# Optimization experiments

Measured on AMD Instinct MI355X. Metric: run time of the kernel, lower is better.

The kernel has to match this reference:

```python
import jax, jax.numpy as jnp
import numpy as np

N = 64          # num_nodes (EEG electrodes)
T = 200         # time steps
B = 64          # batch
H = 64          # hidden_dim
K = 3           # cheb_k
F_IN = 1        # input_dim
D_GRU = 2 * H * N  # 8192, GRU input size


def setup_inputs() -> dict:
    key = jax.random.key(0)
    ks = jax.random.split(key, 24)
    s = 0.05
    inp = {
        "x": jax.random.normal(ks[0], (B, N, T), dtype=jnp.float32),
        "spatial_ei": jax.random.randint(ks[1], (2, 512), 0, N, dtype=jnp.int32),
        "spatial_ew": jax.random.uniform(ks[2], (512,), dtype=jnp.float32),
        "functional_ei": jax.random.randint(ks[3], (2, 1024), 0, N, dtype=jnp.int32),
        "functional_ew": jax.random.uniform(ks[4], (1024,), dtype=jnp.float32),
        # ChebConv: K separate Linear(F_IN->H, bias shared once)
        "Wcheb": jax.random.normal(ks[5], (K, F_IN, H), dtype=jnp.float32) * s,
        "bcheb": jnp.zeros((H,), jnp.float32),
        # GCNConv
        "Wgcn": jax.random.normal(ks[6], (F_IN, H), dtype=jnp.float32) * s,
        "bgcn": jnp.zeros((H,), jnp.float32),
        # bidirectional GRU (torch layout: gates r,z,n stacked -> 3H rows)
        "Wih_f": jax.random.normal(ks[7], (3 * H, D_GRU), dtype=jnp.float32) * s,
        "Whh_f": jax.random.normal(ks[8], (3 * H, H), dtype=jnp.float32) * s,
        "bih_f": jnp.zeros((3 * H,), jnp.float32),
        "bhh_f": jnp.zeros((3 * H,), jnp.float32),
        "Wih_b": jax.random.normal(ks[9], (3 * H, D_GRU), dtype=jnp.float32) * s,
        "Whh_b": jax.random.normal(ks[10], (3 * H, H), dtype=jnp.float32) * s,
        "bih_b": jnp.zeros((3 * H,), jnp.float32),
        "bhh_b": jnp.zeros((3 * H,), jnp.float32),
        # attention + classifier heads
        "attn_W": jax.random.normal(ks[11], (2 * H, 1), dtype=jnp.float32) * s,
        "attn_b": jnp.zeros((1,), jnp.float32),
        "clf_W": jax.random.normal(ks[12], (2 * H, 1), dtype=jnp.float32) * s,
        "clf_b": jnp.zeros((1,), jnp.float32),
    }
    return inp


def _gru_scan(xp, Whh, bhh, reverse):
    # xp: [B, T, 3H] precomputed input projection; returns [B, T, H]
    xp_t = jnp.swapaxes(xp, 0, 1)  # [T, B, 3H]
    Hh = Whh.shape[1]

    def step(h, xg):
        hg = h @ Whh.T + bhh
        xr, xz, xn = jnp.split(xg, 3, axis=-1)
        hr, hz, hn = jnp.split(hg, 3, axis=-1)
        r = jax.nn.sigmoid(xr + hr)
        z = jax.nn.sigmoid(xz + hz)
        n = jnp.tanh(xn + r * hn)
        h_new = (1.0 - z) * n + z * h
        return h_new, h_new

    h0 = jnp.zeros((xp.shape[0], Hh), xp.dtype)
    _, hs = jax.lax.scan(step, h0, xp_t, reverse=reverse)
    return jnp.swapaxes(hs, 0, 1)


def _forward(x, spatial_ei, spatial_ew, functional_ei, functional_ew,
             Wcheb, bcheb, Wgcn, bgcn,
             Wih_f, Whh_f, bih_f, bhh_f, Wih_b, Whh_b, bih_b, bhh_b,
             attn_W, attn_b, clf_W, clf_b):
    x = x[..., None]  # [B, N, T, 1] (the x.dim()==3 -> unsqueeze path)
    Bsz, Nn, Tt, _ = x.shape

    # ---- ChebConv (PyG, sym norm, lambda_max=2): L_tilde = -D^-1/2 A D^-1/2
    # (scaled-Laplacian self loops cancel: 2*1/2 - 1 = 0)
    row, col = spatial_ei[0], spatial_ei[1]
    deg = jax.ops.segment_sum(spatial_ew, row, num_segments=Nn)
    dinv = jnp.where(deg > 0, jax.lax.rsqrt(jnp.where(deg > 0, deg, 1.0)), 0.0)
    wn = dinv[row] * spatial_ew * dinv[col]
    # operator S[i, j]: aggregate source j into target i (source_to_target flow)
    S = jnp.zeros((Nn, Nn), x.dtype).at[col, row].add(wn)
    Ltil = -S
    Tx0 = x
    Tx1 = jnp.einsum('ij,bjtf->bitf', Ltil, Tx0)
    out_s = jnp.einsum('bntf,fh->bnth', Tx0, Wcheb[0]) + jnp.einsum('bntf,fh->bnth', Tx1, Wcheb[1])
    for k in range(2, K):
        Tx2 = 2.0 * jnp.einsum('ij,bjtf->bitf', Ltil, Tx1) - Tx0
        out_s = out_s + jnp.einsum('bntf,fh->bnth', Tx2, Wcheb[k])
        Tx0, Tx1 = Tx1, Tx2
    h_sp = out_s + bcheb  # [B, N, T, H]

    # ---- GCNConv (PyG gcn_norm with self loops, weight 1)
    row, col = functional_ei[0], functional_ei[1]
    deg = jax.ops.segment_sum(functional_ew, col, num_segments=Nn) + 1.0
    dinv = jax.lax.rsqrt(deg)
    wn = dinv[row] * functional_ew * dinv[col]
    Sg = jnp.zeros((Nn, Nn), x.dtype).at[col, row].add(wn) + jnp.diag(dinv * dinv)
    h_fn = jnp.einsum('bntf,fh->bnth', jnp.einsum('ij,bjtf->bitf', Sg, x), Wgcn) + bgcn

    # ---- stack over time, flatten nodes
    h = jnp.concatenate([h_sp, h_fn], axis=-1)           # [B, N, T, 2H]
    gru_in = jnp.transpose(h, (0, 2, 1, 3)).reshape(Bsz, Tt, Nn * 2 * H)

    # ---- bidirectional GRU
    xp_f = jnp.einsum('btd,gd->btg', gru_in, Wih_f) + bih_f
    xp_b = jnp.einsum('btd,gd->btg', gru_in, Wih_b) + bih_b
    h_f = _gru_scan(xp_f, Whh_f, bhh_f, reverse=False)
    h_b = _gru_scan(xp_b, Whh_b, bhh_b, reverse=True)
    gru_out = jnp.concatenate([h_f, h_b], axis=-1)       # [B, T, 2H]

    # ---- attention pooling + classifier
    scores = jnp.tanh(gru_out @ attn_W + attn_b)         # [B, T, 1]
    aw = jax.nn.softmax(scores, axis=1)
    ctx = jnp.sum(aw * gru_out, axis=1)                  # [B, 2H]
    return jax.nn.sigmoid(ctx @ clf_W + clf_b)           # [B, 1]


def reference(x, spatial_ei, spatial_ew, functional_ei, functional_ew,
              Wcheb, bcheb, Wgcn, bgcn,
              Wih_f, Whh_f, bih_f, bhh_f, Wih_b, Whh_b, bih_b, bhh_b,
              attn_W, attn_b, clf_W, clf_b):
    return _forward(x, spatial_ei, spatial_ew, functional_ei, functional_ew,
                    Wcheb, bcheb, Wgcn, bgcn,
                    Wih_f, Whh_f, bih_f, bhh_f, Wih_b, Whh_b, bih_b, bhh_b,
                    attn_W, attn_b, clf_W, clf_b)
```

## Files before the change

### kernel.cpp

```cpp
#include <hip/hip_runtime.h>
#include <math.h>

#define Nn 64
#define Tt 200
#define Bb 64

__device__ __forceinline__ float sigm(float x){ return 1.0f/(1.0f+__expf(-x)); }
__device__ __forceinline__ float tanh_fast(float x){
  x = fminf(fmaxf(x, -15.f), 15.f);
  float e = __expf(-2.f*x);
  return (1.f - e)/(1.f + e);
}

typedef __attribute__((ext_vector_type(2))) _Float16 h2v;
typedef __attribute__((ext_vector_type(4))) float f4;

#if __has_builtin(__builtin_amdgcn_fdot2)
#define DOT2(w,hv,acc) __builtin_amdgcn_fdot2((w),(hv),(acc),false)
#else
#define DOT2(w,hv,acc) fmaf((float)(w)[0],(float)(hv)[0], fmaf((float)(w)[1],(float)(hv)[1],(acc)))
#endif

__global__ __launch_bounds__(256) void k1_graphs(
    const int* __restrict__ sp_ei, const float* __restrict__ sp_ew,
    const int* __restrict__ fn_ei, const float* __restrict__ fn_ew,
    float* __restrict__ Lg, float* __restrict__ L2g, float* __restrict__ Gm)
{
  __shared__ float deg[Nn];
  __shared__ float dinv[Nn];
  __shared__ float S[64*68];
  const int tid = threadIdx.x;

  if (tid < Nn) deg[tid] = 0.f;
  for (int i=tid;i<64*68;i+=256) S[i]=0.f;
  __syncthreads();
  for (int e=tid;e<512;e+=256) atomicAdd(&deg[sp_ei[e]], sp_ew[e]);
  __syncthreads();
  if (tid < Nn) dinv[tid] = (deg[tid] > 0.f) ? rsqrtf(deg[tid]) : 0.f;
  __syncthreads();
  for (int e=tid;e<512;e+=256) {
    int r = sp_ei[e], c = sp_ei[512+e];
    atomicAdd(&S[c*68 + r], dinv[r]*sp_ew[e]*dinv[c]);
  }
  __syncthreads();
  for (int i=tid;i<4096;i+=256) Lg[i] = -S[(i>>6)*68 + (i&63)];
  {
    const int n = tid>>2, mb = (tid&3)*16;
    float a[16];
    #pragma unroll
    for (int q=0;q<16;q++) a[q]=0.f;
    for (int j=0;j<64;j++){
      float snj = S[n*68+j];
      const float4* rj = (const float4*)&S[j*68+mb];
      #pragma unroll
      for (int q=0;q<4;q++){
        float4 v = rj[q];
        a[q*4+0]=fmaf(snj,v.x,a[q*4+0]);
        a[q*4+1]=fmaf(snj,v.y,a[q*4+1]);
        a[q*4+2]=fmaf(snj,v.z,a[q*4+2]);
        a[q*4+3]=fmaf(snj,v.w,a[q*4+3]);
      }
    }
    #pragma unroll
    for (int q=0;q<16;q++){
      int m = mb+q;
      L2g[n*64+m] = 2.f*a[q] - (n==m ? 1.f : 0.f);
    }
  }
  __syncthreads();

  if (tid < Nn) deg[tid] = 0.f;
  for (int i=tid;i<64*68;i+=256) S[i]=0.f;
  __syncthreads();
  for (int e=tid;e<1024;e+=256) atomicAdd(&deg[fn_ei[1024+e]], fn_ew[e]);
  __syncthreads();
  if (tid < Nn) dinv[tid] = rsqrtf(deg[tid] + 1.f);
  __syncthreads();
  for (int e=tid;e<1024;e+=256) {
    int r = fn_ei[e], c = fn_ei[1024+e];
    atomicAdd(&S[c*68 + r], dinv[r]*fn_ew[e]*dinv[c]);
  }
  __syncthreads();
  if (tid < Nn) S[tid*68 + tid] += dinv[tid]*dinv[tid];
  __syncthreads();
  for (int i=tid;i<4096;i+=256) Gm[i] = S[(i>>6)*68 + (i&63)];
}

__global__ __launch_bounds__(64) void k2_aeff(
    const float* __restrict__ Wih_f, const float* __restrict__ bih_f,
    const float* __restrict__ Wih_b, const float* __restrict__ bih_b,
    const float* __restrict__ Wcheb, const float* __restrict__ bcheb,
    const float* __restrict__ Wgcn,  const float* __restrict__ bgcn,
    const float* __restrict__ Lg, const float* __restrict__ L2g,
    const float* __restrict__ Gm,
    float* __restrict__ Aeff, float* __restrict__ constv)
{
  const int g = blockIdx.x;
  const int dir = (g >= 192) ? 1 : 0;
  const int grow = dir ? g - 192 : g;
  const float* Wih = dir ? Wih_b : Wih_f;
  const float* bih = dir ? bih_b : bih_f;

  __shared__ float wrow[64*129];
  __shared__ float arow[256];
  const int tid = threadIdx.x;

  for (int i = tid; i < 8192; i += 64)
    wrow[(i>>7)*129 + (i&127)] = Wih[grow*8192 + i];
  __syncthreads();

  const int n = tid;
  float a0=0.f,a1=0.f,a2=0.f,a3=0.f,cp=0.f;
  for (int c=0;c<64;c++) {
    float w1 = wrow[n*129 + c];
    a0 = fmaf(w1, Wcheb[c],     a0);
    a1 = fmaf(w1, Wcheb[64+c],  a1);
    a2 = fmaf(w1, Wcheb[128+c], a2);
    cp = fmaf(w1, bcheb[c],     cp);
    float w2 = wrow[n*129 + 64 + c];
    a3 = fmaf(w2, Wgcn[c], a3);
    cp = fmaf(w2, bgcn[c], cp);
  }
  arow[n*4+0]=a0; arow[n*4+1]=a1; arow[n*4+2]=a2; arow[n*4+3]=a3;
  for (int off=32; off; off>>=1) cp += __shfl_down(cp, off, 64);
  if (tid==0) constv[g] = cp + bih[grow];
  __syncthreads();

  const int m = tid;
  float ae = arow[m*4+0];
  for (int nn2=0; nn2<64; nn2++) {
    ae = fmaf(arow[nn2*4+1], Lg [nn2*64+m], ae);
    ae = fmaf(arow[nn2*4+2], L2g[nn2*64+m], ae);
    ae = fmaf(arow[nn2*4+3], Gm [nn2*64+m], ae);
  }
  Aeff[g*64+m] = ae;
}

__global__ __launch_bounds__(256) void k4_gemm(
    const float* __restrict__ x, const float* __restrict__ Aeff,
    const float* __restrict__ constv, float* __restrict__ xp)
{
  const int m0 = blockIdx.x*64, g0 = blockIdx.y*64;
  __shared__ float sX[64*68];
  __shared__ float sA[64*68];
  const int tid = threadIdx.x;

  {
    const int row = tid & 63;
    const int kq  = tid >> 6;
    const int m = m0 + row;
    const int b = m / 200;
    const int t = m - b*200;
    const float* xb = x + (size_t)b*64*200 + t;
    #pragma unroll
    for (int kk=0; kk<16; ++kk) {
      int k = kq*16 + kk;
      sX[k*68 + row] = xb[(size_t)k*200];
    }
  }
  {
    const float4* A4 = (const float4*)Aeff;
    #pragma unroll
    for (int i=0;i<4;i++) {
      int f = tid + i*256;
      int r2 = f >> 4, kq2 = f & 15;
      float4 w = A4[(g0+r2)*16 + kq2];
      sA[(kq2*4+0)*68 + r2] = w.x;
      sA[(kq2*4+1)*68 + r2] = w.y;
      sA[(kq2*4+2)*68 + r2] = w.z;
      sA[(kq2*4+3)*68 + r2] = w.w;
    }
  }
  __syncthreads();

  const int tm = tid & 15, tn = tid >> 4;
  float acc[4][4] = {};
  #pragma unroll 8
  for (int k=0;k<64;k++) {
    float4 a  = *(const float4*)&sX[k*68 + tm*4];
    float4 bb = *(const float4*)&sA[k*68 + tn*4];
    float av[4]={a.x,a.y,a.z,a.w}, bv[4]={bb.x,bb.y,bb.z,bb.w};
    #pragma unroll
    for (int i=0;i<4;i++)
      #pragma unroll
      for (int j=0;j<4;j++)
        acc[i][j] = fmaf(av[i], bv[j], acc[i][j]);
  }

  float cv[4];
  #pragma unroll
  for (int j=0;j<4;j++) cv[j] = constv[g0 + tn*4 + j];
  #pragma unroll
  for (int i=0;i<4;i++) {
    int mrow = m0 + tm*4 + i;
    #pragma unroll
    for (int j=0;j<4;j++)
      xp[mrow*384 + g0 + tn*4 + j] = acc[i][j] + cv[j];
  }
}

__global__ __launch_bounds__(64)
__attribute__((amdgpu_waves_per_eu(1, 1)))
void k5_gru(
    const float* __restrict__ xp,
    const float* __restrict__ Whh_f, const float* __restrict__ bhh_f,
    const float* __restrict__ Whh_b, const float* __restrict__ bhh_b,
    float* __restrict__ gru_out)
{
  const int bd = blockIdx.x;
  const int b = bd >> 1, dir = bd & 1;
  const int g = threadIdx.x & 63;
  const float* Whh = dir ? Whh_b : Whh_f;
  const float* bhh = dir ? bhh_b : bhh_f;

  h2v wr[32], wz[32], wn[32];
  #pragma unroll
  for (int i=0;i<32;i++){
    float2 a = ((const float2*)(Whh + (size_t)g*64))[i];
    float2 bq= ((const float2*)(Whh + (size_t)(64+g)*64))[i];
    float2 c = ((const float2*)(Whh + (size_t)(128+g)*64))[i];
    wr[i] = h2v{(_Float16)a.x, (_Float16)a.y};
    wz[i] = h2v{(_Float16)bq.x,(_Float16)bq.y};
    wn[i] = h2v{(_Float16)c.x, (_Float16)c.y};
  }
  const float br_ = bhh[g], bz_ = bhh[64+g], bn_ = bhh[128+g];

  __shared__ __align__(16) _Float16 hsh[64];
  hsh[g] = (_Float16)0.f;

  const int t0 = dir ? (Tt-1) : 0;
  const int tstep = dir ? -1 : 1;
  const float* xb = xp + (size_t)(b*Tt)*384 + dir*192 + g;
  float* gout = gru_out + (size_t)(b*Tt)*128 + dir*64 + g;

  float h = 0.f;
  float xrA = xb[(size_t)t0*384], xzA = xb[(size_t)t0*384+64], xnA = xb[(size_t)t0*384+128];
  const int t1 = t0 + tstep;
  float xrB = xb[(size_t)t1*384], xzB = xb[(size_t)t1*384+64], xnB = xb[(size_t)t1*384+128];

  int t = t0;
  auto STEP = [&](float& xr, float& xz, float& xn){
    const float cxr = xr, cxz = xz, cxn = xn;
    const int tpre = t + 2*tstep;
    if ((unsigned)tpre < (unsigned)Tt) {
      xr = xb[(size_t)tpre*384];
      xz = xb[(size_t)tpre*384+64];
      xn = xb[(size_t)tpre*384+128];
    }

    const uint4* hp4 = (const uint4*)hsh;
    union U { uint4 v; h2v p[4]; };
    float ar0=0.f,ar1=0.f,az0=0.f,az1=0.f,an0=0.f,an1=0.f;

#define DOTS8(U0,U1,base)                                                     \
    { _Pragma("unroll")                                                       \
      for (int j=0;j<4;j++){                                                  \
        ar0=DOT2(wr[(base)+j],  U0.p[j],ar0);                                 \
        az0=DOT2(wz[(base)+j],  U0.p[j],az0);                                 \
        an0=DOT2(wn[(base)+j],  U0.p[j],an0);                                 \
        ar1=DOT2(wr[(base)+4+j],U1.p[j],ar1);                                 \
        az1=DOT2(wz[(base)+4+j],U1.p[j],az1);                                 \
        an1=DOT2(wn[(base)+4+j],U1.p[j],an1);                                 \
      } }

    U A0,A1,B0,B1,C0,C1,D0,D1;
    A0.v=hp4[0]; A1.v=hp4[1]; B0.v=hp4[2]; B1.v=hp4[3];
    __builtin_amdgcn_sched_group_barrier(0x100, 4, 0);
    DOTS8(A0,A1,0);
    __builtin_amdgcn_sched_group_barrier(0x2, 24, 0);
    C0.v=hp4[4]; C1.v=hp4[5];
    __builtin_amdgcn_sched_group_barrier(0x100, 2, 0);
    DOTS8(B0,B1,8);
    __builtin_amdgcn_sched_group_barrier(0x2, 24, 0);
    D0.v=hp4[6]; D1.v=hp4[7];
    __builtin_amdgcn_sched_group_barrier(0x100, 2, 0);
    DOTS8(C0,C1,16);
    __builtin_amdgcn_sched_group_barrier(0x2, 24, 0);
    DOTS8(D0,D1,24);
    __builtin_amdgcn_sched_group_barrier(0x2, 24, 0);
#undef DOTS8

    float r   = sigm(cxr + (ar0+ar1) + br_);
    float z   = sigm(cxz + (az0+az1) + bz_);
    float nn2 = tanh_fast(cxn + r*((an0+an1) + bn_));
    float hnew = (1.f - z)*nn2 + z*h;
    h = hnew;
    hsh[g] = (_Float16)hnew;
    gout[(size_t)t*128] = hnew;
    t += tstep;
  };

  for (int sp=0; sp<Tt; sp+=2) { STEP(xrA,xzA,xnA); STEP(xrB,xzB,xnB); }
}

__global__ __launch_bounds__(256) void k6_attn(
    const float* __restrict__ gru_out,
    const float* __restrict__ attn_W, const float* __restrict__ attn_b,
    const float* __restrict__ clf_W,  const float* __restrict__ clf_b,
    float* __restrict__ out)
{
  const int b = blockIdx.x, tid = threadIdx.x;
  __shared__ float s_s[Tt];
  __shared__ float red[256];
  __shared__ float aW[128], cW[128];
  if (tid < 128) { aW[tid]=attn_W[tid]; cW[tid]=clf_W[tid]; }
  __syncthreads();

  if (tid < Tt) {
    const float* row = gru_out + (b*Tt + tid)*128;
    float acc = 0.f;
    for (int j=0;j<128;j++) acc = fmaf(row[j], aW[j], acc);
    s_s[tid] = tanhf(acc + attn_b[0]);
  }
  __syncthreads();

  red[tid] = (tid < Tt) ? s_s[tid] : -1e30f;
  __syncthreads();
  for (int s2=128;s2;s2>>=1){ if(tid<s2) red[tid]=fmaxf(red[tid],red[tid+s2]); __syncthreads(); }
  float mx = red[0];
  __syncthreads();

  float e = 0.f;
  if (tid < Tt) { e = expf(s_s[tid]-mx); s_s[tid] = e; }
  red[tid] = e;
  __syncthreads();
  for (int s2=128;s2;s2>>=1){ if(tid<s2) red[tid]+=red[tid+s2]; __syncthreads(); }
  float total = red[0];
  __syncthreads();

  float p = 0.f;
  if (tid < 128) {
    float c = 0.f;
    for (int t=0;t<Tt;t++) c = fmaf(s_s[t], gru_out[(b*Tt+t)*128 + tid], c);
    p = (c/total)*cW[tid];
  }
  red[tid] = p;
  __syncthreads();
  for (int s2=128;s2;s2>>=1){ if(tid<s2) red[tid]+=red[tid+s2]; __syncthreads(); }
  if (tid==0) out[b] = sigm(red[0] + clf_b[0]);
}

extern "C" void kernel_launch(void* const* d_in, const int* in_sizes, int n_in,
                              void* d_out, int out_size, void* d_ws, size_t ws_size,
                              hipStream_t stream)
{
  const float* x      = (const float*)d_in[0];
  const int*   sp_ei  = (const int*)  d_in[1];
  const float* sp_ew  = (const float*)d_in[2];
  const int*   fn_ei  = (const int*)  d_in[3];
  const float* fn_ew  = (const float*)d_in[4];
  const float* Wcheb  = (const float*)d_in[5];
  const float* bcheb  = (const float*)d_in[6];
  const float* Wgcn   = (const float*)d_in[7];
  const float* bgcn   = (const float*)d_in[8];
  const float* Wih_f  = (const float*)d_in[9];
  const float* Whh_f  = (const float*)d_in[10];
  const float* bih_f  = (const float*)d_in[11];
  const float* bhh_f  = (const float*)d_in[12];
  const float* Wih_b  = (const float*)d_in[13];
  const float* Whh_b  = (const float*)d_in[14];
  const float* bih_b  = (const float*)d_in[15];
  const float* bhh_b  = (const float*)d_in[16];
  const float* attn_W = (const float*)d_in[17];
  const float* attn_b = (const float*)d_in[18];
  const float* clf_W  = (const float*)d_in[19];
  const float* clf_b  = (const float*)d_in[20];
  float* out = (float*)d_out;

  float* ws     = (float*)d_ws;
  float* Lg     = ws;
  float* L2g    = Lg   + 4096;
  float* Gm     = L2g  + 4096;
  float* Aeff   = Gm   + 4096;
  float* constv = Aeff + 24576;
  float* xp     = constv + 512;
  float* gro    = xp   + 4915200;

  hipLaunchKernelGGL(k1_graphs,    dim3(1),      dim3(256), 0, stream,
                     sp_ei, sp_ew, fn_ei, fn_ew, Lg, L2g, Gm);
  hipLaunchKernelGGL(k2_aeff,      dim3(384),    dim3(64),  0, stream,
                     Wih_f, bih_f, Wih_b, bih_b, Wcheb, bcheb, Wgcn, bgcn,
                     Lg, L2g, Gm, Aeff, constv);
  hipLaunchKernelGGL(k4_gemm,      dim3(200, 6), dim3(256), 0, stream,
                     x, Aeff, constv, xp);
  hipLaunchKernelGGL(k5_gru,       dim3(128),    dim3(64),  0, stream,
                     xp, Whh_f, bhh_f, Whh_b, bhh_b, gro);
  hipLaunchKernelGGL(k6_attn,      dim3(64),     dim3(256), 0, stream,
                     gro, attn_W, attn_b, clf_W, clf_b, out);
}
```

Baseline: 136.9 us.

## Fuse forward and backward GRU directions into one wave per batch

The recurrent kernel now processes both GRU directions for a batch element in a single 64-thread block, holding both directions' hidden weights in registers and interleaving their dot products and gate math each step. This halves the grid and gives the scheduler two independent recurrence chains to overlap, targeting the serial latency of each timestep. It doubles register pressure and per-step instruction count, and it removes the custom sched_group_barrier ordering.

```diff
diff --git a/kernel.cpp b/kernel.cpp
--- a/kernel.cpp
+++ b/kernel.cpp
@@ -207,90 +207,98 @@
     const float* __restrict__ Whh_b, const float* __restrict__ bhh_b,
     float* __restrict__ gru_out)
 {
-  const int bd = blockIdx.x;
-  const int b = bd >> 1, dir = bd & 1;
+  const int b = blockIdx.x;
   const int g = threadIdx.x & 63;
-  const float* Whh = dir ? Whh_b : Whh_f;
-  const float* bhh = dir ? bhh_b : bhh_f;
-
-  h2v wr[32], wz[32], wn[32];
+
+  h2v wrF[32], wzF[32], wnF[32], wrB[32], wzB[32], wnB[32];
   #pragma unroll
   for (int i=0;i<32;i++){
-    float2 a = ((const float2*)(Whh + (size_t)g*64))[i];
-    float2 bq= ((const float2*)(Whh + (size_t)(64+g)*64))[i];
-    float2 c = ((const float2*)(Whh + (size_t)(128+g)*64))[i];
-    wr[i] = h2v{(_Float16)a.x, (_Float16)a.y};
-    wz[i] = h2v{(_Float16)bq.x,(_Float16)bq.y};
-    wn[i] = h2v{(_Float16)c.x, (_Float16)c.y};
-  }
-  const float br_ = bhh[g], bz_ = bhh[64+g], bn_ = bhh[128+g];
-
-  __shared__ __align__(16) _Float16 hsh[64];
-  hsh[g] = (_Float16)0.f;
-
-  const int t0 = dir ? (Tt-1) : 0;
-  const int tstep = dir ? -1 : 1;
-  const float* xb = xp + (size_t)(b*Tt)*384 + dir*192 + g;
-  float* gout = gru_out + (size_t)(b*Tt)*128 + dir*64 + g;
-
-  float h = 0.f;
-  float xrA = xb[(size_t)t0*384], xzA = xb[(size_t)t0*384+64], xnA = xb[(size_t)t0*384+128];
-  const int t1 = t0 + tstep;
-  float xrB = xb[(size_t)t1*384], xzB = xb[(size_t)t1*384+64], xnB = xb[(size_t)t1*384+128];
-
-  int t = t0;
-  auto STEP = [&](float& xr, float& xz, float& xn){
-    const float cxr = xr, cxz = xz, cxn = xn;
-    const int tpre = t + 2*tstep;
-    if ((unsigned)tpre < (unsigned)Tt) {
-      xr = xb[(size_t)tpre*384];
-      xz = xb[(size_t)tpre*384+64];
-      xn = xb[(size_t)tpre*384+128];
-    }
-
-    const uint4* hp4 = (const uint4*)hsh;
+    float2 a = ((const float2*)(Whh_f + (size_t)g*64))[i];
+    float2 c = ((const float2*)(Whh_f + (size_t)(64+g)*64))[i];
+    float2 d = ((const float2*)(Whh_f + (size_t)(128+g)*64))[i];
+    wrF[i] = h2v{(_Float16)a.x, (_Float16)a.y};
+    wzF[i] = h2v{(_Float16)c.x, (_Float16)c.y};
+    wnF[i] = h2v{(_Float16)d.x, (_Float16)d.y};
+    float2 a2 = ((const float2*)(Whh_b + (size_t)g*64))[i];
+    float2 c2 = ((const float2*)(Whh_b + (size_t)(64+g)*64))[i];
+    float2 d2 = ((const float2*)(Whh_b + (size_t)(128+g)*64))[i];
+    wrB[i] = h2v{(_Float16)a2.x, (_Float16)a2.y};
+    wzB[i] = h2v{(_Float16)c2.x, (_Float16)c2.y};
+    wnB[i] = h2v{(_Float16)d2.x, (_Float16)d2.y};
+  }
+  const float brF = bhh_f[g], bzF = bhh_f[64+g], bnF = bhh_f[128+g];
+  const float brB = bhh_b[g], bzB = bhh_b[64+g], bnB = bhh_b[128+g];
+
+  __shared__ __align__(16) _Float16 hshF[64];
+  __shared__ __align__(16) _Float16 hshB[64];
+  hshF[g] = (_Float16)0.f;
+  hshB[g] = (_Float16)0.f;
+
+  const float* xbF = xp + (size_t)(b*Tt)*384 + g;
+  const float* xbB = xp + (size_t)(b*Tt)*384 + 192 + g;
+  float* goF = gru_out + (size_t)(b*Tt)*128 + g;
+  float* goB = gru_out + (size_t)(b*Tt)*128 + 64 + g;
+
+  float hF = 0.f, hB = 0.f;
+  float xrFA = xbF[0],            xzFA = xbF[64],            xnFA = xbF[128];
+  float xrFB = xbF[384],          xzFB = xbF[384+64],        xnFB = xbF[384+128];
+  float xrBA = xbB[(size_t)199*384], xzBA = xbB[(size_t)199*384+64], xnBA = xbB[(size_t)199*384+128];
+  float xrBB = xbB[(size_t)198*384], xzBB = xbB[(size_t)198*384+64], xnBB = xbB[(size_t)198*384+128];
+
+  int tF = 0, tB = Tt-1;
+  auto STEP = [&](float& xrF, float& xzF, float& xnF,
+                  float& xrB, float& xzB, float& xnB){
+    const float cxrF=xrF, cxzF=xzF, cxnF=xnF;
+    const float cxrB=xrB, cxzB=xzB, cxnB=xnB;
+    const int tpF = tF + 2, tpB = tB - 2;
+    if (tpF < Tt) {
+      xrF = xbF[(size_t)tpF*384]; xzF = xbF[(size_t)tpF*384+64]; xnF = xbF[(size_t)tpF*384+128];
+    }
+    if (tpB >= 0) {
+      xrB = xbB[(size_t)tpB*384]; xzB = xbB[(size_t)tpB*384+64]; xnB = xbB[(size_t)tpB*384+128];
+    }
+
+    const uint4* hF4 = (const uint4*)hshF;
+    const uint4* hB4 = (const uint4*)hshB;
     union U { uint4 v; h2v p[4]; };
-    float ar0=0.f,ar1=0.f,az0=0.f,az1=0.f,an0=0.f,an1=0.f;
-
-#define DOTS8(U0,U1,base)                                                     \
-    { _Pragma("unroll")                                                       \
-      for (int j=0;j<4;j++){                                                  \
-        ar0=DOT2(wr[(base)+j],  U0.p[j],ar0);                                 \
-        az0=DOT2(wz[(base)+j],  U0.p[j],az0);                                 \
-        an0=DOT2(wn[(base)+j],  U0.p[j],an0);                                 \
-        ar1=DOT2(wr[(base)+4+j],U1.p[j],ar1);                                 \
-        az1=DOT2(wz[(base)+4+j],U1.p[j],az1);                                 \
-        an1=DOT2(wn[(base)+4+j],U1.p[j],an1);                                 \
-      } }
-
-    U A0,A1,B0,B1,C0,C1,D0,D1;
-    A0.v=hp4[0]; A1.v=hp4[1]; B0.v=hp4[2]; B1.v=hp4[3];
-    __builtin_amdgcn_sched_group_barrier(0x100, 4, 0);
-    DOTS8(A0,A1,0);
-    __builtin_amdgcn_sched_group_barrier(0x2, 24, 0);
-    C0.v=hp4[4]; C1.v=hp4[5];
-    __builtin_amdgcn_sched_group_barrier(0x100, 2, 0);
-    DOTS8(B0,B1,8);
-    __builtin_amdgcn_sched_group_barrier(0x2, 24, 0);
-    D0.v=hp4[6]; D1.v=hp4[7];
-    __builtin_amdgcn_sched_group_barrier(0x100, 2, 0);
-    DOTS8(C0,C1,16);
-    __builtin_amdgcn_sched_group_barrier(0x2, 24, 0);
-    DOTS8(D0,D1,24);
-    __builtin_amdgcn_sched_group_barrier(0x2, 24, 0);
-#undef DOTS8
-
-    float r   = sigm(cxr + (ar0+ar1) + br_);
-    float z   = sigm(cxz + (az0+az1) + bz_);
-    float nn2 = tanh_fast(cxn + r*((an0+an1) + bn_));
-    float hnew = (1.f - z)*nn2 + z*h;
-    h = hnew;
-    hsh[g] = (_Float16)hnew;
-    gout[(size_t)t*128] = hnew;
-    t += tstep;
+    float arF0=0.f,arF1=0.f,azF0=0.f,azF1=0.f,anF0=0.f,anF1=0.f;
+    float arB0=0.f,arB1=0.f,azB0=0.f,azB1=0.f,anB0=0.f,anB1=0.f;
+
+    #pragma unroll
+    for (int c=0;c<4;c++){
+      U F0,F1,B0,B1;
+      F0.v = hF4[2*c]; F1.v = hF4[2*c+1];
+      B0.v = hB4[2*c]; B1.v = hB4[2*c+1];
+      const int base = 8*c;
+      #pragma unroll
+      for (int j=0;j<4;j++){
+        arF0=DOT2(wrF[base+j],  F0.p[j],arF0); azF0=DOT2(wzF[base+j],  F0.p[j],azF0); anF0=DOT2(wnF[base+j],  F0.p[j],anF0);
+        arB0=DOT2(wrB[base+j],  B0.p[j],arB0); azB0=DOT2(wzB[base+j],  B0.p[j],azB0); anB0=DOT2(wnB[base+j],  B0.p[j],anB0);
+        arF1=DOT2(wrF[base+4+j],F1.p[j],arF1); azF1=DOT2(wzF[base+4+j],F1.p[j],azF1); anF1=DOT2(wnF[base+4+j],F1.p[j],anF1);
+        arB1=DOT2(wrB[base+4+j],B1.p[j],arB1); azB1=DOT2(wzB[base+4+j],B1.p[j],azB1); anB1=DOT2(wnB[base+4+j],B1.p[j],anB1);
+      }
+    }
+
+    float rF  = sigm(cxrF + (arF0+arF1) + brF);
+    float rB  = sigm(cxrB + (arB0+arB1) + brB);
+    float zF  = sigm(cxzF + (azF0+azF1) + bzF);
+    float zB  = sigm(cxzB + (azB0+azB1) + bzB);
+    float nF  = tanh_fast(cxnF + rF*((anF0+anF1) + bnF));
+    float nB  = tanh_fast(cxnB + rB*((anB0+anB1) + bnB));
+    float hnF = (1.f - zF)*nF + zF*hF;
+    float hnB = (1.f - zB)*nB + zB*hB;
+    hF = hnF; hB = hnB;
+    hshF[g] = (_Float16)hnF;
+    hshB[g] = (_Float16)hnB;
+    goF[(size_t)tF*128] = hnF;
+    goB[(size_t)tB*128] = hnB;
+    tF++; tB--;
   };
 
-  for (int sp=0; sp<Tt; sp+=2) { STEP(xrA,xzA,xnA); STEP(xrB,xzB,xnB); }
+  for (int sp=0; sp<Tt; sp+=2) {
+    STEP(xrFA,xzFA,xnFA, xrBA,xzBA,xnBA);
+    STEP(xrFB,xzFB,xnFB, xrBB,xzBB,xnBB);
+  }
 }
 
 __global__ __launch_bounds__(256) void k6_attn(
@@ -383,7 +391,7 @@
                      Lg, L2g, Gm, Aeff, constv);
   hipLaunchKernelGGL(k4_gemm,      dim3(200, 6), dim3(256), 0, stream,
                      x, Aeff, constv, xp);
-  hipLaunchKernelGGL(k5_gru,       dim3(128),    dim3(64),  0, stream,
+  hipLaunchKernelGGL(k5_gru,       dim3(64),     dim3(64),  0, stream,
                      xp, Whh_f, bhh_f, Whh_b, bhh_b, gro);
   hipLaunchKernelGGL(k6_attn,      dim3(64),     dim3(256), 0, stream,
                      gro, attn_W, attn_b, clf_W, clf_b, out);
```

Measured after the change: 242.6 us. +77.3%, slower.

## Process two batch sequences per GRU wavefront to interleave independent recurrences

Applied to the files above, without the earlier changes.

Each GRU block now runs two batch elements for the same direction, with separate shared-memory hidden-state buffers, and the grid is halved from 128 to 64 blocks. The two independent recurrences are interleaved in one instruction stream so their dot-product and activation latencies can overlap within a wave, and the register-held weights are reused for both. The explicit sched_group_barrier scheduling hints are dropped. In exchange, per-step instruction count doubles per wave and fewer CUs are used, so the serial step time may grow.

```diff
diff --git a/kernel.cpp b/kernel.cpp
--- a/kernel.cpp
+++ b/kernel.cpp
@@ -207,8 +207,9 @@
     const float* __restrict__ Whh_b, const float* __restrict__ bhh_b,
     float* __restrict__ gru_out)
 {
-  const int bd = blockIdx.x;
-  const int b = bd >> 1, dir = bd & 1;
+  const int bid = blockIdx.x;
+  const int dir = bid & 1;
+  const int b0 = (bid >> 1)*2, b1 = b0 + 1;
   const int g = threadIdx.x & 63;
   const float* Whh = dir ? Whh_b : Whh_f;
   const float* bhh = dir ? bhh_b : bhh_f;
@@ -225,72 +226,77 @@
   }
   const float br_ = bhh[g], bz_ = bhh[64+g], bn_ = bhh[128+g];
 
-  __shared__ __align__(16) _Float16 hsh[64];
-  hsh[g] = (_Float16)0.f;
+  __shared__ __align__(16) _Float16 h0sh[64];
+  __shared__ __align__(16) _Float16 h1sh[64];
+  h0sh[g] = (_Float16)0.f;
+  h1sh[g] = (_Float16)0.f;
 
   const int t0 = dir ? (Tt-1) : 0;
   const int tstep = dir ? -1 : 1;
-  const float* xb = xp + (size_t)(b*Tt)*384 + dir*192 + g;
-  float* gout = gru_out + (size_t)(b*Tt)*128 + dir*64 + g;
-
-  float h = 0.f;
-  float xrA = xb[(size_t)t0*384], xzA = xb[(size_t)t0*384+64], xnA = xb[(size_t)t0*384+128];
-  const int t1 = t0 + tstep;
-  float xrB = xb[(size_t)t1*384], xzB = xb[(size_t)t1*384+64], xnB = xb[(size_t)t1*384+128];
+  const float* xb0 = xp + (size_t)(b0*Tt)*384 + dir*192 + g;
+  const float* xb1 = xp + (size_t)(b1*Tt)*384 + dir*192 + g;
+  float* go0 = gru_out + (size_t)(b0*Tt)*128 + dir*64 + g;
+  float* go1 = gru_out + (size_t)(b1*Tt)*128 + dir*64 + g;
+
+  float h0 = 0.f, h1 = 0.f;
+  const int t1i = t0 + tstep;
+  float x0rA = xb0[(size_t)t0*384],  x0zA = xb0[(size_t)t0*384+64],  x0nA = xb0[(size_t)t0*384+128];
+  float x0rB = xb0[(size_t)t1i*384], x0zB = xb0[(size_t)t1i*384+64], x0nB = xb0[(size_t)t1i*384+128];
+  float x1rA = xb1[(size_t)t0*384],  x1zA = xb1[(size_t)t0*384+64],  x1nA = xb1[(size_t)t0*384+128];
+  float x1rB = xb1[(size_t)t1i*384], x1zB = xb1[(size_t)t1i*384+64], x1nB = xb1[(size_t)t1i*384+128];
 
   int t = t0;
-  auto STEP = [&](float& xr, float& xz, float& xn){
-    const float cxr = xr, cxz = xz, cxn = xn;
+  auto STEP = [&](float& x0r, float& x0z, float& x0n,
+                  float& x1r, float& x1z, float& x1n){
+    const float c0r=x0r, c0z=x0z, c0n=x0n;
+    const float c1r=x1r, c1z=x1z, c1n=x1n;
     const int tpre = t + 2*tstep;
     if ((unsigned)tpre < (unsigned)Tt) {
-      xr = xb[(size_t)tpre*384];
-      xz = xb[(size_t)tpre*384+64];
-      xn = xb[(size_t)tpre*384+128];
-    }
-
-    const uint4* hp4 = (const uint4*)hsh;
+      x0r = xb0[(size_t)tpre*384]; x0z = xb0[(size_t)tpre*384+64]; x0n = xb0[(size_t)tpre*384+128];
+      x1r = xb1[(size_t)tpre*384]; x1z = xb1[(size_t)tpre*384+64]; x1n = xb1[(size_t)tpre*384+128];
+    }
+
+    const uint4* h04 = (const uint4*)h0sh;
+    const uint4* h14 = (const uint4*)h1sh;
     union U { uint4 v; h2v p[4]; };
-    float ar0=0.f,ar1=0.f,az0=0.f,az1=0.f,an0=0.f,an1=0.f;
-
-#define DOTS8(U0,U1,base)                                                     \
-    { _Pragma("unroll")                                                       \
-      for (int j=0;j<4;j++){                                                  \
-        ar0=DOT2(wr[(base)+j],  U0.p[j],ar0);                                 \
-        az0=DOT2(wz[(base)+j],  U0.p[j],az0);                                 \
-        an0=DOT2(wn[(base)+j],  U0.p[j],an0);                                 \
-        ar1=DOT2(wr[(base)+4+j],U1.p[j],ar1);                                 \
-        az1=DOT2(wz[(base)+4+j],U1.p[j],az1);                                 \
-        an1=DOT2(wn[(base)+4+j],U1.p[j],an1);                                 \
-      } }
-
-    U A0,A1,B0,B1,C0,C1,D0,D1;
-    A0.v=hp4[0]; A1.v=hp4[1]; B0.v=hp4[2]; B1.v=hp4[3];
-    __builtin_amdgcn_sched_group_barrier(0x100, 4, 0);
-    DOTS8(A0,A1,0);
-    __builtin_amdgcn_sched_group_barrier(0x2, 24, 0);
-    C0.v=hp4[4]; C1.v=hp4[5];
-    __builtin_amdgcn_sched_group_barrier(0x100, 2, 0);
-    DOTS8(B0,B1,8);
-    __builtin_amdgcn_sched_group_barrier(0x2, 24, 0);
-    D0.v=hp4[6]; D1.v=hp4[7];
-    __builtin_amdgcn_sched_group_barrier(0x100, 2, 0);
-    DOTS8(C0,C1,16);
-    __builtin_amdgcn_sched_group_barrier(0x2, 24, 0);
-    DOTS8(D0,D1,24);
-    __builtin_amdgcn_sched_group_barrier(0x2, 24, 0);
-#undef DOTS8
-
-    float r   = sigm(cxr + (ar0+ar1) + br_);
-    float z   = sigm(cxz + (az0+az1) + bz_);
-    float nn2 = tanh_fast(cxn + r*((an0+an1) + bn_));
-    float hnew = (1.f - z)*nn2 + z*h;
-    h = hnew;
-    hsh[g] = (_Float16)hnew;
-    gout[(size_t)t*128] = hnew;
+    float a0r0=0.f,a0r1=0.f,a0z0=0.f,a0z1=0.f,a0n0=0.f,a0n1=0.f;
+    float a1r0=0.f,a1r1=0.f,a1z0=0.f,a1z1=0.f,a1n0=0.f,a1n1=0.f;
+
+    #pragma unroll
+    for (int c=0;c<4;c++){
+      U F0,F1,G0,G1;
+      F0.v = h04[2*c]; F1.v = h04[2*c+1];
+      G0.v = h14[2*c]; G1.v = h14[2*c+1];
+      const int base = 8*c;
+      #pragma unroll
+      for (int j=0;j<4;j++){
+        a0r0=DOT2(wr[base+j],  F0.p[j],a0r0); a0z0=DOT2(wz[base+j],  F0.p[j],a0z0); a0n0=DOT2(wn[base+j],  F0.p[j],a0n0);
+        a1r0=DOT2(wr[base+j],  G0.p[j],a1r0); a1z0=DOT2(wz[base+j],  G0.p[j],a1z0); a1n0=DOT2(wn[base+j],  G0.p[j],a1n0);
+        a0r1=DOT2(wr[base+4+j],F1.p[j],a0r1); a0z1=DOT2(wz[base+4+j],F1.p[j],a0z1); a0n1=DOT2(wn[base+4+j],F1.p[j],a0n1);
+        a1r1=DOT2(wr[base+4+j],G1.p[j],a1r1); a1z1=DOT2(wz[base+4+j],G1.p[j],a1z1); a1n1=DOT2(wn[base+4+j],G1.p[j],a1n1);
+      }
+    }
+
+    float r0  = sigm(c0r + (a0r0+a0r1) + br_);
+    float r1  = sigm(c1r + (a1r0+a1r1) + br_);
+    float z0  = sigm(c0z + (a0z0+a0z1) + bz_);
+    float z1  = sigm(c1z + (a1z0+a1z1) + bz_);
+    float n0  = tanh_fast(c0n + r0*((a0n0+a0n1) + bn_));
+    float n1  = tanh_fast(c1n + r1*((a1n0+a1n1) + bn_));
+    float hn0 = (1.f - z0)*n0 + z0*h0;
+    float hn1 = (1.f - z1)*n1 + z1*h1;
+    h0 = hn0; h1 = hn1;
+    h0sh[g] = (_Float16)hn0;
+    h1sh[g] = (_Float16)hn1;
+    go0[(size_t)t*128] = hn0;
+    go1[(size_t)t*128] = hn1;
     t += tstep;
   };
 
-  for (int sp=0; sp<Tt; sp+=2) { STEP(xrA,xzA,xnA); STEP(xrB,xzB,xnB); }
+  for (int sp=0; sp<Tt; sp+=2) {
+    STEP(x0rA,x0zA,x0nA, x1rA,x1zA,x1nA);
+    STEP(x0rB,x0zB,x0nB, x1rB,x1zB,x1nB);
+  }
 }
 
 __global__ __launch_bounds__(256) void k6_attn(
@@ -383,7 +389,7 @@
                      Lg, L2g, Gm, Aeff, constv);
   hipLaunchKernelGGL(k4_gemm,      dim3(200, 6), dim3(256), 0, stream,
                      x, Aeff, constv, xp);
-  hipLaunchKernelGGL(k5_gru,       dim3(128),    dim3(64),  0, stream,
+  hipLaunchKernelGGL(k5_gru,       dim3(64),     dim3(64),  0, stream,
                      xp, Whh_f, bhh_f, Whh_b, bhh_b, gro);
   hipLaunchKernelGGL(k6_attn,      dim3(64),     dim3(256), 0, stream,
                      gro, attn_W, attn_b, clf_W, clf_b, out);
```

Result: slower. 208.9 us (+52.6%).

## Pack eight GRU sequences per workgroup and load hidden state upfront

Applied to the files above, without the earlier changes.

The GRU recurrence kernel now runs 8 independent (batch, direction) sequences as separate waves inside one 512-thread block, so it launches 16 blocks instead of 128 single-wave blocks. Each wave keeps its own hidden-state slice in shared memory. The manual sched_group_barrier interleaving of LDS loads and dot products is replaced by loading the whole fp16 hidden vector into registers first, then running a plain unrolled dot loop. The packing concentrates the serial recurrences on 16 compute units, which risks contention on the SIMDs. Dropping the hand-tuned load/compute overlap may also lengthen each time step.

```diff
diff --git a/kernel.cpp b/kernel.cpp
--- a/kernel.cpp
+++ b/kernel.cpp
@@ -199,17 +199,18 @@
   }
 }
 
-__global__ __launch_bounds__(64)
-__attribute__((amdgpu_waves_per_eu(1, 1)))
+__global__ __launch_bounds__(512)
+__attribute__((amdgpu_waves_per_eu(2, 2)))
 void k5_gru(
     const float* __restrict__ xp,
     const float* __restrict__ Whh_f, const float* __restrict__ bhh_f,
     const float* __restrict__ Whh_b, const float* __restrict__ bhh_b,
     float* __restrict__ gru_out)
 {
-  const int bd = blockIdx.x;
-  const int b = bd >> 1, dir = bd & 1;
-  const int g = threadIdx.x & 63;
+  const int wid = threadIdx.x >> 6;
+  const int g   = threadIdx.x & 63;
+  const int sid = blockIdx.x*8 + wid;
+  const int b = sid >> 1, dir = sid & 1;
   const float* Whh = dir ? Whh_b : Whh_f;
   const float* bhh = dir ? bhh_b : bhh_f;
 
@@ -225,8 +226,8 @@
   }
   const float br_ = bhh[g], bz_ = bhh[64+g], bn_ = bhh[128+g];
 
-  __shared__ __align__(16) _Float16 hsh[64];
-  hsh[g] = (_Float16)0.f;
+  __shared__ __align__(16) _Float16 hsh[8][64];
+  hsh[wid][g] = (_Float16)0.f;
 
   const int t0 = dir ? (Tt-1) : 0;
   const int tstep = dir ? -1 : 1;
@@ -238,8 +239,20 @@
   const int t1 = t0 + tstep;
   float xrB = xb[(size_t)t1*384], xzB = xb[(size_t)t1*384+64], xnB = xb[(size_t)t1*384+128];
 
+  _Float16* myh = &hsh[wid][0];
   int t = t0;
   auto STEP = [&](float& xr, float& xz, float& xn){
+    h2v hv[32];
+    {
+      const uint4* hp4 = (const uint4*)myh;
+      #pragma unroll
+      for (int q=0;q<8;q++){
+        union { uint4 v; h2v p[4]; } uu;
+        uu.v = hp4[q];
+        hv[q*4+0]=uu.p[0]; hv[q*4+1]=uu.p[1]; hv[q*4+2]=uu.p[2]; hv[q*4+3]=uu.p[3];
+      }
+    }
+
     const float cxr = xr, cxz = xz, cxn = xn;
     const int tpre = t + 2*tstep;
     if ((unsigned)tpre < (unsigned)Tt) {
@@ -248,44 +261,19 @@
       xn = xb[(size_t)tpre*384+128];
     }
 
-    const uint4* hp4 = (const uint4*)hsh;
-    union U { uint4 v; h2v p[4]; };
     float ar0=0.f,ar1=0.f,az0=0.f,az1=0.f,an0=0.f,an1=0.f;
-
-#define DOTS8(U0,U1,base)                                                     \
-    { _Pragma("unroll")                                                       \
-      for (int j=0;j<4;j++){                                                  \
-        ar0=DOT2(wr[(base)+j],  U0.p[j],ar0);                                 \
-        az0=DOT2(wz[(base)+j],  U0.p[j],az0);                                 \
-        an0=DOT2(wn[(base)+j],  U0.p[j],an0);                                 \
-        ar1=DOT2(wr[(base)+4+j],U1.p[j],ar1);                                 \
-        az1=DOT2(wz[(base)+4+j],U1.p[j],az1);                                 \
-        an1=DOT2(wn[(base)+4+j],U1.p[j],an1);                                 \
-      } }
-
-    U A0,A1,B0,B1,C0,C1,D0,D1;
-    A0.v=hp4[0]; A1.v=hp4[1]; B0.v=hp4[2]; B1.v=hp4[3];
-    __builtin_amdgcn_sched_group_barrier(0x100, 4, 0);
-    DOTS8(A0,A1,0);
-    __builtin_amdgcn_sched_group_barrier(0x2, 24, 0);
-    C0.v=hp4[4]; C1.v=hp4[5];
-    __builtin_amdgcn_sched_group_barrier(0x100, 2, 0);
-    DOTS8(B0,B1,8);
-    __builtin_amdgcn_sched_group_barrier(0x2, 24, 0);
-    D0.v=hp4[6]; D1.v=hp4[7];
-    __builtin_amdgcn_sched_group_barrier(0x100, 2, 0);
-    DOTS8(C0,C1,16);
-    __builtin_amdgcn_sched_group_barrier(0x2, 24, 0);
-    DOTS8(D0,D1,24);
-    __builtin_amdgcn_sched_group_barrier(0x2, 24, 0);
-#undef DOTS8
+    #pragma unroll
+    for (int i=0;i<32;i+=2){
+      ar0 = DOT2(wr[i],  hv[i],  ar0);  az0 = DOT2(wz[i],  hv[i],  az0);  an0 = DOT2(wn[i],  hv[i],  an0);
+      ar1 = DOT2(wr[i+1],hv[i+1],ar1);  az1 = DOT2(wz[i+1],hv[i+1],az1);  an1 = DOT2(wn[i+1],hv[i+1],an1);
+    }
 
     float r   = sigm(cxr + (ar0+ar1) + br_);
     float z   = sigm(cxz + (az0+az1) + bz_);
     float nn2 = tanh_fast(cxn + r*((an0+an1) + bn_));
     float hnew = (1.f - z)*nn2 + z*h;
     h = hnew;
-    hsh[g] = (_Float16)hnew;
+    myh[g] = (_Float16)hnew;
     gout[(size_t)t*128] = hnew;
     t += tstep;
   };
@@ -383,7 +371,7 @@
                      Lg, L2g, Gm, Aeff, constv);
   hipLaunchKernelGGL(k4_gemm,      dim3(200, 6), dim3(256), 0, stream,
                      x, Aeff, constv, xp);
-  hipLaunchKernelGGL(k5_gru,       dim3(128),    dim3(64),  0, stream,
+  hipLaunchKernelGGL(k5_gru,       dim3(16),     dim3(512), 0, stream,
                      xp, Whh_f, bhh_f, Whh_b, bhh_b, gro);
   hipLaunchKernelGGL(k6_attn,      dim3(64),     dim3(256), 0, stream,
                      gro, attn_W, attn_b, clf_W, clf_b, out);
```

After: 202.4 us. 1.48x slower.
